# Optimization experiments

Hardware: AMD Instinct MI355X
Metric: run time of the kernel (lower is better)

Reference implementation:

```python
import jax, jax.numpy as jnp
import numpy as np

N_HEADS = 12
NEG_INF = -1e9


def rotate_half(x):
    x1, x2 = jnp.split(x, 2, axis=-1)
    return jnp.concatenate((-x2, x1), axis=-1)


def rope_tables(T, D, dtype):
    # matches RotaryEmbedding buffers: emb = cat(freqs, freqs), shape [1,1,T,D]
    inv_freq = 1.0 / (10000.0 ** (jnp.arange(0, D, 2, dtype=jnp.float32) / D))
    t = jnp.arange(T, dtype=jnp.float32)
    freqs = jnp.einsum('i,j->ij', t, inv_freq)
    emb = jnp.concatenate((freqs, freqs), axis=-1)
    return jnp.cos(emb)[None, None].astype(dtype), jnp.sin(emb)[None, None].astype(dtype)


def setup_inputs() -> dict:
    key = jax.random.key(0)
    ks = jax.random.split(key, 5)
    B, T, C = 4, 2048, 768
    s = 1.0 / np.sqrt(C)
    x = jax.random.normal(ks[0], (B, T, C), dtype=jnp.float32)
    wq = jax.random.normal(ks[1], (C, C), dtype=jnp.float32) * s
    wk = jax.random.normal(ks[2], (C, C), dtype=jnp.float32) * s
    wv = jax.random.normal(ks[3], (C, C), dtype=jnp.float32) * s
    wo = jax.random.normal(ks[4], (C, C), dtype=jnp.float32) * s
    causal = jnp.tril(jnp.ones((T, T), dtype=bool))
    mask = jnp.where(causal, 0.0, NEG_INF).astype(jnp.float32)[None, None]
    return {"x": x, "wq": wq, "wk": wk, "wv": wv, "wo": wo, "mask": mask}


def reference(x, wq, wk, wv, wo, mask):
    B, T, C = x.shape
    H = N_HEADS
    D = C // H
    # QKV projections (no bias), reshape to [B,H,T,D]
    def proj(w):
        return (x @ w).reshape(B, T, H, D).transpose(0, 2, 1, 3)
    q, k, v = proj(wq), proj(wk), proj(wv)
    cos, sin = rope_tables(T, D, x.dtype)
    q = q * cos + rotate_half(q) * sin
    k = k * cos + rotate_half(k) * sin
    attn = jnp.einsum('bhqd,bhkd->bhqk', q, k) / jnp.sqrt(jnp.asarray(D, x.dtype))
    attn = attn + mask
    attn = jax.nn.softmax(attn, axis=-1)  # dropout = identity (eval mode)
    out = jnp.einsum('bhqk,bhkd->bhqd', attn, v)
    out = out.transpose(0, 2, 1, 3).reshape(B, T, C)
    return out @ wo
```

## Files before the change

### kernel.cpp

```cpp
#include <hip/hip_runtime.h>
#include <hip/hip_bf16.h>
#include <cmath>

typedef _Float16 f16x8 __attribute__((ext_vector_type(8)));
typedef _Float16 f16x4 __attribute__((ext_vector_type(4)));
typedef float f32x4 __attribute__((ext_vector_type(4)));
using h2_t = decltype(__builtin_amdgcn_cvt_pkrtz(0.f, 0.f));

#define T_SEQ 2048
#define C_DIM 768
#define H_NUM 12
#define NX (8192 * 768)
#define NW (768 * 768)

__device__ __forceinline__ unsigned short f2h(float f) {
    _Float16 h = (_Float16)f;
    return __builtin_bit_cast(unsigned short, h);
}

__device__ __forceinline__ float fexp2(float x) {
#if __has_builtin(__builtin_amdgcn_exp2f)
    return __builtin_amdgcn_exp2f(x);
#else
    return exp2f(x);
#endif
}

__device__ __forceinline__ unsigned int pkrtz(float a, float b) {
    auto r = __builtin_amdgcn_cvt_pkrtz(a, b);
    return __builtin_bit_cast(unsigned int, r);
}

__device__ __forceinline__ f16x4 mk4(h2_t a, h2_t b) {
    uint2 u;
    u.x = __builtin_bit_cast(unsigned int, a);
    u.y = __builtin_bit_cast(unsigned int, b);
    return __builtin_bit_cast(f16x4, u);
}

__device__ __forceinline__ float dot2acc(h2_t d, h2_t o, float acc) {
#if __has_builtin(__builtin_amdgcn_fdot2)
    return __builtin_amdgcn_fdot2(d, o, acc, false);
#else
    return acc + (float)d[0] + (float)d[1];
#endif
}

__device__ __forceinline__ void gld16(const unsigned short* g, unsigned short* l) {
    __builtin_amdgcn_global_load_lds(
        (const __attribute__((address_space(1))) unsigned int*)g,
        (__attribute__((address_space(3))) unsigned int*)l, 16, 0, 0);
}

__global__ __launch_bounds__(256)
void prep(const float* __restrict__ x,
          const float* __restrict__ w0, const float* __restrict__ w1,
          const float* __restrict__ w2, const float* __restrict__ w3,
          unsigned short* __restrict__ xb, unsigned short* __restrict__ wt) {
    __shared__ float T[64][65];
    const int pid = blockIdx.x;
    if (pid < 3072) {
        int cidx = pid * 256 + threadIdx.x;
        int row = cidx / 96;
        int cp = cidx - row * 96;
        int dchunk = row * 96 + (cp & ~3) + ((cp & 3) ^ (row & 3));
        const float* s = x + (size_t)cidx * 8;
        float4 v0 = *(const float4*)s, v1 = *(const float4*)(s + 4);
        ushort4 a, b;
        a.x = f2h(v0.x); a.y = f2h(v0.y); a.z = f2h(v0.z); a.w = f2h(v0.w);
        b.x = f2h(v1.x); b.y = f2h(v1.y); b.z = f2h(v1.z); b.w = f2h(v1.w);
        unsigned short* d = xb + (size_t)dchunk * 8;
        *(ushort4*)d = a;
        *(ushort4*)(d + 4) = b;
    } else {
        int t = pid - 3072;
        int z = t / 144, r = t - z * 144;
        int kx = r / 12, ny = r - kx * 12;
        const float* src = (z == 0) ? w0 : (z == 1) ? w1 : (z == 2) ? w2 : w3;
        unsigned short* dst = wt + (size_t)z * NW;
        const int k0 = kx * 64, n0 = ny * 64;
        const int tid = threadIdx.x;
        {
            int rowb = tid >> 4, c4 = (tid & 15) * 4;
#pragma unroll
            for (int i = 0; i < 4; ++i) {
                int row = rowb + i * 16;
                float4 v = *(const float4*)&src[(size_t)(k0 + row) * C_DIM + n0 + c4];
                T[row][c4] = v.x; T[row][c4 + 1] = v.y; T[row][c4 + 2] = v.z; T[row][c4 + 3] = v.w;
            }
        }
        __syncthreads();
        {
            int n = tid & 63, kseg = (tid >> 6) * 16;
            int n_glob = n0 + n;
            unsigned short tmp[16];
#pragma unroll
            for (int j = 0; j < 16; ++j) tmp[j] = f2h(T[kseg + j][n]);
            int base = k0 + (kseg & 32);
            int sub = (kseg >> 3) & 3;
            unsigned short* drow = dst + (size_t)n_glob * C_DIM + base;
            *(uint4*)&drow[(sub ^ (n_glob & 3)) << 3]       = *(uint4*)&tmp[0];
            *(uint4*)&drow[((sub + 1) ^ (n_glob & 3)) << 3] = *(uint4*)&tmp[8];
        }
    }
}

__global__ __launch_bounds__(256, 4)
void qkv_gemm(const unsigned short* __restrict__ xb,
              const unsigned short* __restrict__ wt,
              unsigned short* __restrict__ q_ws,
              unsigned short* __restrict__ k_ws,
              unsigned short* __restrict__ vt_ws) {
    const int pid = blockIdx.x;
    const int xcd = pid & 7, idx = pid >> 3;
    const int mloc = idx / 18, nw = idx - mloc * 18;
    const int which = nw % 3, nx = nw / 3;
    const unsigned short* W = wt + (size_t)which * NW;
    const int n0 = nx * 128, m0 = (xcd * 8 + mloc) * 128;

    __shared__ __align__(16) unsigned short As[8192];
    __shared__ __align__(16) unsigned short Bs[8192];

    const int tid = threadIdx.x, lane = tid & 63, w = tid >> 6;
    const int quad = lane >> 4, l16 = lane & 15;
    const int wm = (w >> 1) * 64, wn = (w & 1) * 64;

    f32x4 acc[4][4] = {};

    for (int k0 = 0; k0 < C_DIM; k0 += 64) {
        __syncthreads();
#pragma unroll
        for (int c = 0; c < 4; ++c) {
            int e = c * 256 + tid;
            int p = e >> 9, row = (e >> 2) & 127, ch = e & 3;
            int kc = k0 + p * 32 + ch * 8;
            gld16(xb + (size_t)(m0 + row) * C_DIM + kc, &As[e * 8]);
            gld16(W  + (size_t)(n0 + row) * C_DIM + kc, &Bs[e * 8]);
        }
        __syncthreads();
#pragma unroll
        for (int p = 0; p < 2; ++p) {
            f16x8 af[4], bf[4];
#pragma unroll
            for (int mt = 0; mt < 4; ++mt) {
                int r = wm + mt * 16 + l16;
                af[mt] = *(const f16x8*)&As[p * 4096 + r * 32 + ((quad ^ (r & 3)) << 3)];
            }
#pragma unroll
            for (int nt = 0; nt < 4; ++nt) {
                int r = wn + nt * 16 + l16;
                bf[nt] = *(const f16x8*)&Bs[p * 4096 + r * 32 + ((quad ^ (r & 3)) << 3)];
            }
#pragma unroll
            for (int mt = 0; mt < 4; ++mt)
#pragma unroll
                for (int nt = 0; nt < 4; ++nt)
                    acc[mt][nt] = __builtin_amdgcn_mfma_f32_16x16x32_f16(af[mt], bf[nt], acc[mt][nt], 0, 0, 0);
        }
    }

    const int head = nx * 2 + (w & 1);

    if (which < 2) {
        unsigned short* dst = (which == 0) ? q_ws : k_ws;
        const float qscale = 0.18033688011112042f;
#pragma unroll
        for (int ntp = 0; ntp < 2; ++ntp) {
            int d1 = ntp * 16 + l16;
            float invf = __expf(-0.28782313662425572f * (float)d1);
#pragma unroll
            for (int mt = 0; mt < 4; ++mt)
#pragma unroll
                for (int reg = 0; reg < 4; ++reg) {
                    int m = m0 + wm + mt * 16 + quad * 4 + reg;
                    int t = m & (T_SEQ - 1), bb = m >> 11;
                    float sn, cs;
                    __sincosf((float)t * invf, &sn, &cs);
                    float v1 = acc[mt][ntp][reg], v2 = acc[mt][ntp + 2][reg];
                    float o1 = v1 * cs - v2 * sn;
                    float o2 = v2 * cs + v1 * sn;
                    if (which == 0) { o1 *= qscale; o2 *= qscale; }
                    size_t o = ((size_t)(bb * H_NUM + head) * T_SEQ + t) * 64 + d1;
                    dst[o] = f2h(o1);
                    dst[o + 32] = f2h(o2);
                }
        }
    } else {
#pragma unroll
        for (int nt = 0; nt < 4; ++nt) {
            int d = nt * 16 + l16;
#pragma unroll
            for (int mt = 0; mt < 4; ++mt) {
                int m = m0 + wm + mt * 16 + quad * 4;
                int t = m & (T_SEQ - 1), bb = m >> 11;
                ushort4 pk;
                pk.x = f2h(acc[mt][nt][0]); pk.y = f2h(acc[mt][nt][1]);
                pk.z = f2h(acc[mt][nt][2]); pk.w = f2h(acc[mt][nt][3]);
                *(ushort4*)&vt_ws[((size_t)(bb * H_NUM + head) * 64 + d) * T_SEQ + t] = pk;
            }
        }
    }
}

__global__ __launch_bounds__(256, 3)
void flash_attn(const unsigned short* __restrict__ q_ws,
                const unsigned short* __restrict__ k_ws,
                const unsigned short* __restrict__ vt_ws,
                unsigned short* __restrict__ attn_out) {
    __shared__ __align__(16) unsigned short Kbuf[2][64 * 64];
    __shared__ __align__(16) unsigned short Vbuf[2][64 * 64];

    const int pid = blockIdx.x;
    const int xcd = pid & 7, slot = pid >> 3;
    const int bh_l = slot >> 4;
    const int bh = xcd * 6 + bh_l;
    const int pr = (slot + 3 * bh_l) & 15;
    const int qa = pr, qb = 31 - pr;
    const int b = bh / H_NUM, h = bh % H_NUM;

    const int tid = threadIdx.x, lane = tid & 63, w = tid >> 6;
    const int quad = lane >> 4, l16 = lane & 15;
    const size_t base = (size_t)bh * (T_SEQ * 64);

    const unsigned short* qAp = q_ws + base + (size_t)(qa * 64 + w * 16 + l16) * 64 + quad * 8;
    f16x8 aqA0 = *(const f16x8*)(qAp);
    f16x8 aqA1 = *(const f16x8*)(qAp + 32);
    const unsigned short* qBp = q_ws + base + (size_t)(qb * 64 + w * 16 + l16) * 64 + quad * 8;
    f16x8 aqB0 = *(const f16x8*)(qBp);
    f16x8 aqB1 = *(const f16x8*)(qBp + 32);

    f32x4 accA[4] = {}, accB[4] = {};
    float laccA = 0.f, laccB = 0.f;
    const h2_t ones2 = __builtin_amdgcn_cvt_pkrtz(1.f, 1.f);

    const int r_in = lane >> 3;
    const int cpr = lane & 7;
    const int gch = (cpr ^ r_in) * 8;

#define DMA_KV(P, KT)                                                                  \
    {                                                                                  \
        _Pragma("unroll")                                                              \
        for (int j = 0; j < 2; ++j) {                                                  \
            int row = w * 16 + j * 8 + r_in;                                           \
            gld16(k_ws + base + (size_t)((KT) * 64 + row) * 64 + gch,                  \
                  &Kbuf[P][(w * 16 + j * 8) * 64]);                                    \
            gld16(vt_ws + base + (size_t)row * T_SEQ + (KT) * 64 + gch,                \
                  &Vbuf[P][(w * 16 + j * 8) * 64]);                                    \
        }                                                                              \
    }

    const int fo = (quad ^ (l16 & 7)) << 3;

    const int q1 = quad >> 1, q0 = quad & 1, s7 = l16 & 7;
    int voff[4];
#pragma unroll
    for (int kb = 0; kb < 4; ++kb)
        voff[kb] = (((((kb << 1) | q1) ^ s7) << 3) | (q0 << 2));

    DMA_KV(0, 0);
    for (int kt = 0; kt <= qb; ++kt) {
        const int cur = kt & 1;
        __syncthreads();
        if (kt < qb) DMA_KV(cur ^ 1, kt + 1);
        const int doA = (kt <= qa);

        f16x8 bk[4][2];
#pragma unroll
        for (int nt = 0; nt < 4; ++nt) {
            const unsigned short* kr = &Kbuf[cur][(nt * 16 + l16) * 64 + fo];
            bk[nt][0] = *(const f16x8*)(kr);
            bk[nt][1] = *(const f16x8*)((const unsigned short*)((size_t)kr ^ 64));
        }

        f32x4 sB[4] = {}, sA[4] = {};
        __builtin_amdgcn_s_setprio(1);
#pragma unroll
        for (int nt = 0; nt < 4; ++nt) {
            sB[nt] = __builtin_amdgcn_mfma_f32_16x16x32_f16(bk[nt][0], aqB0, sB[nt], 0, 0, 0);
            sB[nt] = __builtin_amdgcn_mfma_f32_16x16x32_f16(bk[nt][1], aqB1, sB[nt], 0, 0, 0);
        }
        if (doA) {
#pragma unroll
            for (int nt = 0; nt < 4; ++nt) {
                sA[nt] = __builtin_amdgcn_mfma_f32_16x16x32_f16(bk[nt][0], aqA0, sA[nt], 0, 0, 0);
                sA[nt] = __builtin_amdgcn_mfma_f32_16x16x32_f16(bk[nt][1], aqA1, sA[nt], 0, 0, 0);
            }
        }
        __builtin_amdgcn_s_setprio(0);

        if (kt == qb) {
#pragma unroll
            for (int nt = 0; nt < 4; ++nt)
#pragma unroll
                for (int reg = 0; reg < 4; ++reg)
                    if (nt * 16 + quad * 4 + reg > w * 16 + l16) sB[nt][reg] = -1e30f;
        }
        if (kt == qa) {
#pragma unroll
            for (int nt = 0; nt < 4; ++nt)
#pragma unroll
                for (int reg = 0; reg < 4; ++reg)
                    if (nt * 16 + quad * 4 + reg > w * 16 + l16) sA[nt][reg] = -1e30f;
        }

        f16x4 pbB[4], pbA[4];
#pragma unroll
        for (int kb = 0; kb < 4; ++kb) {
            float p0 = fexp2(sB[kb][0]), p1 = fexp2(sB[kb][1]);
            float p2 = fexp2(sB[kb][2]), p3 = fexp2(sB[kb][3]);
            h2_t d0 = __builtin_amdgcn_cvt_pkrtz(p0, p1);
            h2_t d1 = __builtin_amdgcn_cvt_pkrtz(p2, p3);
            laccB = dot2acc(d0, ones2, laccB);
            laccB = dot2acc(d1, ones2, laccB);
            pbB[kb] = mk4(d0, d1);
        }
        if (doA) {
#pragma unroll
            for (int kb = 0; kb < 4; ++kb) {
                float p0 = fexp2(sA[kb][0]), p1 = fexp2(sA[kb][1]);
                float p2 = fexp2(sA[kb][2]), p3 = fexp2(sA[kb][3]);
                h2_t d0 = __builtin_amdgcn_cvt_pkrtz(p0, p1);
                h2_t d1 = __builtin_amdgcn_cvt_pkrtz(p2, p3);
                laccA = dot2acc(d0, ones2, laccA);
                laccA = dot2acc(d1, ones2, laccA);
                pbA[kb] = mk4(d0, d1);
            }
        }

        __builtin_amdgcn_s_setprio(1);
#pragma unroll
        for (int ntd = 0; ntd < 4; ++ntd) {
            const unsigned short* vrow = &Vbuf[cur][(ntd * 16 + l16) * 64];
            f16x4 av0 = *(const f16x4*)(vrow + voff[0]);
            f16x4 av1 = *(const f16x4*)(vrow + voff[1]);
            f16x4 av2 = *(const f16x4*)(vrow + voff[2]);
            f16x4 av3 = *(const f16x4*)(vrow + voff[3]);
            accB[ntd] = __builtin_amdgcn_mfma_f32_16x16x16f16(av0, pbB[0], accB[ntd], 0, 0, 0);
            accB[ntd] = __builtin_amdgcn_mfma_f32_16x16x16f16(av1, pbB[1], accB[ntd], 0, 0, 0);
            accB[ntd] = __builtin_amdgcn_mfma_f32_16x16x16f16(av2, pbB[2], accB[ntd], 0, 0, 0);
            accB[ntd] = __builtin_amdgcn_mfma_f32_16x16x16f16(av3, pbB[3], accB[ntd], 0, 0, 0);
            if (doA) {
                accA[ntd] = __builtin_amdgcn_mfma_f32_16x16x16f16(av0, pbA[0], accA[ntd], 0, 0, 0);
                accA[ntd] = __builtin_amdgcn_mfma_f32_16x16x16f16(av1, pbA[1], accA[ntd], 0, 0, 0);
                accA[ntd] = __builtin_amdgcn_mfma_f32_16x16x16f16(av2, pbA[2], accA[ntd], 0, 0, 0);
                accA[ntd] = __builtin_amdgcn_mfma_f32_16x16x16f16(av3, pbA[3], accA[ntd], 0, 0, 0);
            }
        }
        __builtin_amdgcn_s_setprio(0);
    }
#undef DMA_KV

    laccB += __shfl_xor(laccB, 16);
    laccB += __shfl_xor(laccB, 32);
    laccA += __shfl_xor(laccA, 16);
    laccA += __shfl_xor(laccA, 32);
    const float rB = 1.0f / laccB;
    const float rA = 1.0f / laccA;

    const int tB = qb * 64 + w * 16 + l16;
    const int tA = qa * 64 + w * 16 + l16;
#pragma unroll
    for (int ntd = 0; ntd < 4; ++ntd) {
        int col = h * 64 + ntd * 16 + quad * 4;
        ushort4 pkB;
        pkB.x = f2h(accB[ntd][0] * rB); pkB.y = f2h(accB[ntd][1] * rB);
        pkB.z = f2h(accB[ntd][2] * rB); pkB.w = f2h(accB[ntd][3] * rB);
        *(ushort4*)&attn_out[(size_t)(b * T_SEQ + tB) * C_DIM + col] = pkB;
        ushort4 pkA;
        pkA.x = f2h(accA[ntd][0] * rA); pkA.y = f2h(accA[ntd][1] * rA);
        pkA.z = f2h(accA[ntd][2] * rA); pkA.w = f2h(accA[ntd][3] * rA);
        *(ushort4*)&attn_out[(size_t)(b * T_SEQ + tA) * C_DIM + col] = pkA;
    }
}

__global__ __launch_bounds__(256, 4)
void out_proj(const unsigned short* __restrict__ ab,
              const unsigned short* __restrict__ wt_o,
              float* __restrict__ out) {
    const int pid = blockIdx.x;
    const int xcd = pid & 7, idx = pid >> 3;
    const int mloc = idx / 12, nx = idx - mloc * 12;
    const int n0 = nx * 64, m0 = (xcd * 8 + mloc) * 128;

    __shared__ __align__(16) unsigned short As[8192];
    __shared__ __align__(16) unsigned short Bs[4096];

    const int tid = threadIdx.x, lane = tid & 63, w = tid >> 6;
    const int quad = lane >> 4, l16 = lane & 15;
    const int wm = w * 32;

    f32x4 acc[2][4] = {};
    const int srow = tid >> 1, shalf = tid & 1;

    for (int k0 = 0; k0 < C_DIM; k0 += 64) {
        __syncthreads();
#pragma unroll
        for (int p = 0; p < 2; ++p) {
            const unsigned short* g = ab + (size_t)(m0 + srow) * C_DIM + k0 + p * 32 + shalf * 16;
            uint4 d0 = *(const uint4*)g;
            uint4 d1 = *(const uint4*)(g + 8);
            *(uint4*)&As[p * 4096 + srow * 32 + (((shalf * 2 + 0) ^ (srow & 3)) << 3)] = d0;
            *(uint4*)&As[p * 4096 + srow * 32 + (((shalf * 2 + 1) ^ (srow & 3)) << 3)] = d1;
        }
#pragma unroll
        for (int c = 0; c < 2; ++c) {
            int e = c * 256 + tid;
            int p = e >> 8, row = (e >> 2) & 63, ch = e & 3;
            gld16(wt_o + (size_t)(n0 + row) * C_DIM + k0 + p * 32 + ch * 8, &Bs[e * 8]);
        }
        __syncthreads();
#pragma unroll
        for (int p = 0; p < 2; ++p) {
            f16x8 af[2], bf[4];
#pragma unroll
            for (int mt = 0; mt < 2; ++mt) {
                int r = wm + mt * 16 + l16;
                af[mt] = *(const f16x8*)&As[p * 4096 + r * 32 + ((quad ^ (r & 3)) << 3)];
            }
#pragma unroll
            for (int nt = 0; nt < 4; ++nt) {
                int r = nt * 16 + l16;
                bf[nt] = *(const f16x8*)&Bs[p * 2048 + r * 32 + ((quad ^ (r & 3)) << 3)];
            }
#pragma unroll
            for (int mt = 0; mt < 2; ++mt)
#pragma unroll
                for (int nt = 0; nt < 4; ++nt)
                    acc[mt][nt] = __builtin_amdgcn_mfma_f32_16x16x32_f16(af[mt], bf[nt], acc[mt][nt], 0, 0, 0);
        }
    }

#pragma unroll
    for (int mt = 0; mt < 2; ++mt)
#pragma unroll
        for (int nt = 0; nt < 4; ++nt)
#pragma unroll
            for (int reg = 0; reg < 4; ++reg) {
                int m = m0 + wm + mt * 16 + quad * 4 + reg;
                int n = n0 + nt * 16 + l16;
                out[(size_t)m * C_DIM + n] = acc[mt][nt][reg];
            }
}

extern "C" void kernel_launch(void* const* d_in, const int* in_sizes, int n_in,
                              void* d_out, int out_size, void* d_ws, size_t ws_size,
                              hipStream_t stream) {
    const float* x  = (const float*)d_in[0];
    const float* wq = (const float*)d_in[1];
    const float* wk = (const float*)d_in[2];
    const float* wv = (const float*)d_in[3];
    const float* wo = (const float*)d_in[4];
    float* out = (float*)d_out;

    unsigned short* xb    = (unsigned short*)d_ws;
    unsigned short* wt    = xb + NX;
    unsigned short* q_ws  = wt + 4 * (size_t)NW;
    unsigned short* k_ws  = q_ws + NX;
    unsigned short* vt_ws = k_ws + NX;
    unsigned short* attn  = xb;

    prep<<<3648, 256, 0, stream>>>(x, wq, wk, wv, wo, xb, wt);
    qkv_gemm<<<1152, 256, 0, stream>>>(xb, wt, q_ws, k_ws, vt_ws);
    flash_attn<<<768, 256, 0, stream>>>(q_ws, k_ws, vt_ws, attn);
    out_proj<<<768, 256, 0, stream>>>(attn, wt + 3 * (size_t)NW, out);
}
```

Measured before the change: 214.4 us.

## Split paired query strips into one strip per block, longest first

Each flash-attention block previously processed two query strips (qa and 31-qa) that shared the K/V tiles staged in LDS, which balanced the causal workload. Now each block handles a single strip, the grid doubles to 1536 blocks, strips are issued longest first, and launch bounds allow 5 blocks per CU. This cuts registers per block and raises occupancy, and the descending order is meant to balance the tail. In exchange every K/V tile is loaded from memory twice as often, since paired strips no longer share it.

```diff
diff --git a/kernel.cpp b/kernel.cpp
--- a/kernel.cpp
+++ b/kernel.cpp
@@ -24,11 +24,6 @@
 #else
     return exp2f(x);
 #endif
-}
-
-__device__ __forceinline__ unsigned int pkrtz(float a, float b) {
-    auto r = __builtin_amdgcn_cvt_pkrtz(a, b);
-    return __builtin_bit_cast(unsigned int, r);
 }
 
 __device__ __forceinline__ f16x4 mk4(h2_t a, h2_t b) {
@@ -202,7 +197,7 @@
     }
 }
 
-__global__ __launch_bounds__(256, 3)
+__global__ __launch_bounds__(256, 5)
 void flash_attn(const unsigned short* __restrict__ q_ws,
                 const unsigned short* __restrict__ k_ws,
                 const unsigned short* __restrict__ vt_ws,
@@ -212,25 +207,21 @@
 
     const int pid = blockIdx.x;
     const int xcd = pid & 7, slot = pid >> 3;
-    const int bh_l = slot >> 4;
-    const int bh = xcd * 6 + bh_l;
-    const int pr = (slot + 3 * bh_l) & 15;
-    const int qa = pr, qb = 31 - pr;
+    const int sdiv = slot / 6;
+    const int strip = 31 - sdiv;
+    const int bh = xcd * 6 + (slot - sdiv * 6);
     const int b = bh / H_NUM, h = bh % H_NUM;
 
     const int tid = threadIdx.x, lane = tid & 63, w = tid >> 6;
     const int quad = lane >> 4, l16 = lane & 15;
     const size_t base = (size_t)bh * (T_SEQ * 64);
 
-    const unsigned short* qAp = q_ws + base + (size_t)(qa * 64 + w * 16 + l16) * 64 + quad * 8;
-    f16x8 aqA0 = *(const f16x8*)(qAp);
-    f16x8 aqA1 = *(const f16x8*)(qAp + 32);
-    const unsigned short* qBp = q_ws + base + (size_t)(qb * 64 + w * 16 + l16) * 64 + quad * 8;
-    f16x8 aqB0 = *(const f16x8*)(qBp);
-    f16x8 aqB1 = *(const f16x8*)(qBp + 32);
-
-    f32x4 accA[4] = {}, accB[4] = {};
-    float laccA = 0.f, laccB = 0.f;
+    const unsigned short* qp = q_ws + base + (size_t)(strip * 64 + w * 16 + l16) * 64 + quad * 8;
+    f16x8 aq0 = *(const f16x8*)(qp);
+    f16x8 aq1 = *(const f16x8*)(qp + 32);
+
+    f32x4 acc[4] = {};
+    float lacc = 0.f;
     const h2_t ones2 = __builtin_amdgcn_cvt_pkrtz(1.f, 1.f);
 
     const int r_in = lane >> 3;
@@ -258,11 +249,10 @@
         voff[kb] = (((((kb << 1) | q1) ^ s7) << 3) | (q0 << 2));
 
     DMA_KV(0, 0);
-    for (int kt = 0; kt <= qb; ++kt) {
+    for (int kt = 0; kt <= strip; ++kt) {
         const int cur = kt & 1;
         __syncthreads();
-        if (kt < qb) DMA_KV(cur ^ 1, kt + 1);
-        const int doA = (kt <= qa);
+        if (kt < strip) DMA_KV(cur ^ 1, kt + 1);
 
         f16x8 bk[4][2];
 #pragma unroll
@@ -272,59 +262,33 @@
             bk[nt][1] = *(const f16x8*)((const unsigned short*)((size_t)kr ^ 64));
         }
 
-        f32x4 sB[4] = {}, sA[4] = {};
+        f32x4 s[4] = {};
         __builtin_amdgcn_s_setprio(1);
 #pragma unroll
         for (int nt = 0; nt < 4; ++nt) {
-            sB[nt] = __builtin_amdgcn_mfma_f32_16x16x32_f16(bk[nt][0], aqB0, sB[nt], 0, 0, 0);
-            sB[nt] = __builtin_amdgcn_mfma_f32_16x16x32_f16(bk[nt][1], aqB1, sB[nt], 0, 0, 0);
-        }
-        if (doA) {
-#pragma unroll
-            for (int nt = 0; nt < 4; ++nt) {
-                sA[nt] = __builtin_amdgcn_mfma_f32_16x16x32_f16(bk[nt][0], aqA0, sA[nt], 0, 0, 0);
-                sA[nt] = __builtin_amdgcn_mfma_f32_16x16x32_f16(bk[nt][1], aqA1, sA[nt], 0, 0, 0);
-            }
+            s[nt] = __builtin_amdgcn_mfma_f32_16x16x32_f16(bk[nt][0], aq0, s[nt], 0, 0, 0);
+            s[nt] = __builtin_amdgcn_mfma_f32_16x16x32_f16(bk[nt][1], aq1, s[nt], 0, 0, 0);
         }
         __builtin_amdgcn_s_setprio(0);
 
-        if (kt == qb) {
+        if (kt == strip) {
 #pragma unroll
             for (int nt = 0; nt < 4; ++nt)
 #pragma unroll
                 for (int reg = 0; reg < 4; ++reg)
-                    if (nt * 16 + quad * 4 + reg > w * 16 + l16) sB[nt][reg] = -1e30f;
-        }
-        if (kt == qa) {
-#pragma unroll
-            for (int nt = 0; nt < 4; ++nt)
-#pragma unroll
-                for (int reg = 0; reg < 4; ++reg)
-                    if (nt * 16 + quad * 4 + reg > w * 16 + l16) sA[nt][reg] = -1e30f;
-        }
-
-        f16x4 pbB[4], pbA[4];
+                    if (nt * 16 + quad * 4 + reg > w * 16 + l16) s[nt][reg] = -1e30f;
+        }
+
+        f16x4 pb[4];
 #pragma unroll
         for (int kb = 0; kb < 4; ++kb) {
-            float p0 = fexp2(sB[kb][0]), p1 = fexp2(sB[kb][1]);
-            float p2 = fexp2(sB[kb][2]), p3 = fexp2(sB[kb][3]);
+            float p0 = fexp2(s[kb][0]), p1 = fexp2(s[kb][1]);
+            float p2 = fexp2(s[kb][2]), p3 = fexp2(s[kb][3]);
             h2_t d0 = __builtin_amdgcn_cvt_pkrtz(p0, p1);
             h2_t d1 = __builtin_amdgcn_cvt_pkrtz(p2, p3);
-            laccB = dot2acc(d0, ones2, laccB);
-            laccB = dot2acc(d1, ones2, laccB);
-            pbB[kb] = mk4(d0, d1);
-        }
-        if (doA) {
-#pragma unroll
-            for (int kb = 0; kb < 4; ++kb) {
-                float p0 = fexp2(sA[kb][0]), p1 = fexp2(sA[kb][1]);
-                float p2 = fexp2(sA[kb][2]), p3 = fexp2(sA[kb][3]);
-                h2_t d0 = __builtin_amdgcn_cvt_pkrtz(p0, p1);
-                h2_t d1 = __builtin_amdgcn_cvt_pkrtz(p2, p3);
-                laccA = dot2acc(d0, ones2, laccA);
-                laccA = dot2acc(d1, ones2, laccA);
-                pbA[kb] = mk4(d0, d1);
-            }
+            lacc = dot2acc(d0, ones2, lacc);
+            lacc = dot2acc(d1, ones2, lacc);
+            pb[kb] = mk4(d0, d1);
         }
 
         __builtin_amdgcn_s_setprio(1);
@@ -335,41 +299,27 @@
             f16x4 av1 = *(const f16x4*)(vrow + voff[1]);
             f16x4 av2 = *(const f16x4*)(vrow + voff[2]);
             f16x4 av3 = *(const f16x4*)(vrow + voff[3]);
-            accB[ntd] = __builtin_amdgcn_mfma_f32_16x16x16f16(av0, pbB[0], accB[ntd], 0, 0, 0);
-            accB[ntd] = __builtin_amdgcn_mfma_f32_16x16x16f16(av1, pbB[1], accB[ntd], 0, 0, 0);
-            accB[ntd] = __builtin_amdgcn_mfma_f32_16x16x16f16(av2, pbB[2], accB[ntd], 0, 0, 0);
-            accB[ntd] = __builtin_amdgcn_mfma_f32_16x16x16f16(av3, pbB[3], accB[ntd], 0, 0, 0);
-            if (doA) {
-                accA[ntd] = __builtin_amdgcn_mfma_f32_16x16x16f16(av0, pbA[0], accA[ntd], 0, 0, 0);
-                accA[ntd] = __builtin_amdgcn_mfma_f32_16x16x16f16(av1, pbA[1], accA[ntd], 0, 0, 0);
-                accA[ntd] = __builtin_amdgcn_mfma_f32_16x16x16f16(av2, pbA[2], accA[ntd], 0, 0, 0);
-                accA[ntd] = __builtin_amdgcn_mfma_f32_16x16x16f16(av3, pbA[3], accA[ntd], 0, 0, 0);
-            }
+            acc[ntd] = __builtin_amdgcn_mfma_f32_16x16x16f16(av0, pb[0], acc[ntd], 0, 0, 0);
+            acc[ntd] = __builtin_amdgcn_mfma_f32_16x16x16f16(av1, pb[1], acc[ntd], 0, 0, 0);
+            acc[ntd] = __builtin_amdgcn_mfma_f32_16x16x16f16(av2, pb[2], acc[ntd], 0, 0, 0);
+            acc[ntd] = __builtin_amdgcn_mfma_f32_16x16x16f16(av3, pb[3], acc[ntd], 0, 0, 0);
         }
         __builtin_amdgcn_s_setprio(0);
     }
 #undef DMA_KV
 
-    laccB += __shfl_xor(laccB, 16);
-    laccB += __shfl_xor(laccB, 32);
-    laccA += __shfl_xor(laccA, 16);
-    laccA += __shfl_xor(laccA, 32);
-    const float rB = 1.0f / laccB;
-    const float rA = 1.0f / laccA;
-
-    const int tB = qb * 64 + w * 16 + l16;
-    const int tA = qa * 64 + w * 16 + l16;
+    lacc += __shfl_xor(lacc, 16);
+    lacc += __shfl_xor(lacc, 32);
+    const float r = 1.0f / lacc;
+
+    const int t = strip * 64 + w * 16 + l16;
 #pragma unroll
     for (int ntd = 0; ntd < 4; ++ntd) {
         int col = h * 64 + ntd * 16 + quad * 4;
-        ushort4 pkB;
-        pkB.x = f2h(accB[ntd][0] * rB); pkB.y = f2h(accB[ntd][1] * rB);
-        pkB.z = f2h(accB[ntd][2] * rB); pkB.w = f2h(accB[ntd][3] * rB);
-        *(ushort4*)&attn_out[(size_t)(b * T_SEQ + tB) * C_DIM + col] = pkB;
-        ushort4 pkA;
-        pkA.x = f2h(accA[ntd][0] * rA); pkA.y = f2h(accA[ntd][1] * rA);
-        pkA.z = f2h(accA[ntd][2] * rA); pkA.w = f2h(accA[ntd][3] * rA);
-        *(ushort4*)&attn_out[(size_t)(b * T_SEQ + tA) * C_DIM + col] = pkA;
+        ushort4 pk;
+        pk.x = f2h(acc[ntd][0] * r); pk.y = f2h(acc[ntd][1] * r);
+        pk.z = f2h(acc[ntd][2] * r); pk.w = f2h(acc[ntd][3] * r);
+        *(ushort4*)&attn_out[(size_t)(b * T_SEQ + t) * C_DIM + col] = pk;
     }
 }
 
@@ -461,6 +411,6 @@
 
     prep<<<3648, 256, 0, stream>>>(x, wq, wk, wv, wo, xb, wt);
     qkv_gemm<<<1152, 256, 0, stream>>>(xb, wt, q_ws, k_ws, vt_ws);
-    flash_attn<<<768, 256, 0, stream>>>(q_ws, k_ws, vt_ws, attn);
+    flash_attn<<<1536, 256, 0, stream>>>(q_ws, k_ws, vt_ws, attn);
     out_proj<<<768, 256, 0, stream>>>(attn, wt + 3 * (size_t)NW, out);
 }
```

Measured after the change: 209.8 us (median of 3 runs). -2.2%, faster.
